# Kernel tuning notes

Measured on AMD Instinct MI355X. Metric: run time of the kernel, lower is better.

Reference implementation:

```python
import jax, jax.numpy as jnp
import numpy as np

NUM_EMBEDDINGS = 16384
EMBEDDING_DIM = 512
COMMITMENT_COST = 0.25  # legacy: vq_loss = commit + beta * codebook
NORM_EPS = 1e-12  # F.normalize default eps


def setup_inputs() -> dict:
    key = jax.random.key(0)
    k_z, k_emb, k_w, k_b = jax.random.split(key, 4)
    z = jax.random.normal(k_z, (8, 1024, EMBEDDING_DIM), dtype=jnp.float32)
    # frozen codebook, init normal with std = D^{-0.5}
    embedding_weight = jax.random.normal(k_emb, (NUM_EMBEDDINGS, EMBEDDING_DIM), dtype=jnp.float32) * (EMBEDDING_DIM ** -0.5)
    # learnable projection (torch Linear: y = x @ W.T + b, W is [out, in])
    bound = 1.0 / np.sqrt(EMBEDDING_DIM)
    proj_w = jax.random.uniform(k_w, (EMBEDDING_DIM, EMBEDDING_DIM), dtype=jnp.float32, minval=-bound, maxval=bound)
    proj_b = jax.random.uniform(k_b, (EMBEDDING_DIM,), dtype=jnp.float32, minval=-bound, maxval=bound)
    scale = jnp.asarray(10.0, dtype=jnp.float32)
    return {"z": z, "embedding_weight": embedding_weight, "proj_w": proj_w, "proj_b": proj_b, "scale": scale}


def _l2_normalize(x):
    n = jnp.linalg.norm(x, axis=-1, keepdims=True)
    return x / jnp.maximum(n, NORM_EPS)


def reference(z, embedding_weight, proj_w, proj_b, scale):
    B, N, D = z.shape
    z_flat = z.reshape(-1, D)                                   # [M, D]
    quant_codebook = embedding_weight @ proj_w.T + proj_b       # [K, D]
    z_n = _l2_normalize(z_flat)
    c_n = _l2_normalize(quant_codebook)
    distances = -(z_n @ c_n.T) * scale                          # [M, K]
    encoding_indices = jnp.argmin(distances, axis=1)            # [M]
    quantized = quant_codebook[encoding_indices].reshape(z.shape)
    commitment_loss = jnp.mean((jax.lax.stop_gradient(quantized) - z) ** 2)
    codebook_loss = jnp.mean((quantized - jax.lax.stop_gradient(z)) ** 2)
    vq_loss = commitment_loss + COMMITMENT_COST * codebook_loss  # legacy=True
    quantized = z + jax.lax.stop_gradient(quantized - z)         # straight-through
    encoding_indices = encoding_indices.reshape(B, N)
    return quantized, vq_loss, encoding_indices
```

## Files before the change

kernel.cpp:

```cpp
#include <hip/hip_runtime.h>
#include <math.h>


typedef _Float16 f16;
typedef _Float16 f16x8 __attribute__((ext_vector_type(8)));
typedef _Float16 f16x4 __attribute__((ext_vector_type(4)));
typedef short s16x8 __attribute__((ext_vector_type(8)));
typedef float f32x4 __attribute__((ext_vector_type(4)));
typedef unsigned int u32;
typedef unsigned long long u64;
typedef unsigned short ushort_t;

#define INV2048 (1.0f/2048.0f)
#define MARGIN  0.010f

#define OFF_Q    0u
#define OFF_EHI  33554432u
#define OFF_ELO  50331648u
#define OFF_WHI  67108864u
#define OFF_WLO  67633152u
#define OFF_CB   68157440u
#define OFF_ZB   84934656u
#define OFF_RL   93323264u
#define OFF_PK   OFF_EHI

__device__ __forceinline__ void gload_lds16(const void* g, void* l) {
  __builtin_amdgcn_global_load_lds(
      (const __attribute__((address_space(1))) u32*)g,
      (__attribute__((address_space(3))) u32*)l, 16, 0, 0);
}

__device__ __forceinline__ void stage_tile(const void* __restrict__ src, int row0,
                                           int kt, char* lds, int tid) {
#pragma unroll
  for (int i = 0; i < 4; ++i) {
    int lin = i * 256 + tid;
    int row = lin >> 3;
    int slot = lin & 7;
    int k8 = slot ^ (row & 7);
    const char* g = (const char*)src + (((size_t)(row0 + row)) << 10)
                    + (size_t)(kt * 128 + k8 * 16);
    gload_lds16(g, lds + lin * 16);
  }
}

__device__ __forceinline__ u64 make_key(float v, int idx) {
  u32 b = __float_as_uint(v);
  u32 m = (u32)((int)b >> 31) | 0x80000000u;
  return ((u64)(b ^ m) << 32) | (u32)(0x7FFFFFFF - idx);
}
__device__ __forceinline__ float key_val(u64 k) {
  u32 o = (u32)(k >> 32);
  u32 m = (o & 0x80000000u) ? 0x80000000u : 0xFFFFFFFFu;
  return __uint_as_float(o ^ m);
}
__device__ __forceinline__ int key_idx(u64 k) {
  return 0x7FFFFFFF - (int)(u32)(k & 0xFFFFFFFFu);
}
__device__ __forceinline__ u64 umax64(u64 a, u64 b) { return a > b ? a : b; }

#define LDS_AHI 0
#define LDS_ALO 16384
#define LDS_BHI 32768
#define LDS_BLO 49152

__global__ __launch_bounds__(256, 2) void k_gemm_codebook(
    const f16* __restrict__ Ahi, const f16* __restrict__ Alo,
    const f16* __restrict__ Bhi, const f16* __restrict__ Blo,
    const float* __restrict__ bias, float* __restrict__ Q) {
  __shared__ __align__(16) char lds[65536];
  f32x4 hh[4][4], xx[4][4];
  const int tid = threadIdx.x;
  const int m0 = blockIdx.y * 128;
  const int n0 = blockIdx.x * 128;
  const int l = tid & 63;
  const int wid = tid >> 6;
  const int wr = (wid >> 1) * 64;
  const int wc = (wid & 1) * 64;
  const int r7 = (l & 15) & 7;

#pragma unroll
  for (int a = 0; a < 4; ++a)
#pragma unroll
    for (int b = 0; b < 4; ++b) {
      hh[a][b] = (f32x4){0.f, 0.f, 0.f, 0.f};
      xx[a][b] = (f32x4){0.f, 0.f, 0.f, 0.f};
    }

  for (int kt = 0; kt < 8; ++kt) {
    stage_tile(Ahi, m0, kt, lds + LDS_AHI, tid);
    stage_tile(Alo, m0, kt, lds + LDS_ALO, tid);
    stage_tile(Bhi, n0, kt, lds + LDS_BHI, tid);
    stage_tile(Blo, n0, kt, lds + LDS_BLO, tid);
    __syncthreads();
#pragma unroll
    for (int ks = 0; ks < 2; ++ks) {
      const int kg = ks * 4 + (l >> 4);
      const int s = (kg ^ r7) * 16;
      const char* pa = lds + (wr + (l & 15)) * 128 + s;
      const char* pb = lds + (wc + (l & 15)) * 128 + s;
      f16x8 ahi[4], alo[4];
#pragma unroll
      for (int mf = 0; mf < 4; ++mf) {
        ahi[mf] = *(const f16x8*)(pa + LDS_AHI + mf * 2048);
        alo[mf] = *(const f16x8*)(pa + LDS_ALO + mf * 2048);
      }
#pragma unroll
      for (int nf = 0; nf < 4; ++nf) {
        f16x8 bhi = *(const f16x8*)(pb + LDS_BHI + nf * 2048);
        f16x8 blo = *(const f16x8*)(pb + LDS_BLO + nf * 2048);
#pragma unroll
        for (int mf = 0; mf < 4; ++mf) {
          hh[mf][nf] = __builtin_amdgcn_mfma_f32_16x16x32_f16(ahi[mf], bhi, hh[mf][nf], 0, 0, 0);
          xx[mf][nf] = __builtin_amdgcn_mfma_f32_16x16x32_f16(ahi[mf], blo, xx[mf][nf], 0, 0, 0);
          xx[mf][nf] = __builtin_amdgcn_mfma_f32_16x16x32_f16(alo[mf], bhi, xx[mf][nf], 0, 0, 0);
        }
      }
    }
    __syncthreads();
  }

#pragma unroll
  for (int mf = 0; mf < 4; ++mf)
#pragma unroll
    for (int nf = 0; nf < 4; ++nf)
#pragma unroll
      for (int j = 0; j < 4; ++j) {
        int row = m0 + wr + mf * 16 + (l >> 4) * 4 + j;
        int col = n0 + wc + nf * 16 + (l & 15);
        Q[(size_t)row * 512 + col] = hh[mf][nf][j] + xx[mf][nf][j] * INV2048 + bias[col];
      }
}

__global__ __launch_bounds__(256, 4) void k_gemm_coarse(
    const ushort_t* __restrict__ CB, const ushort_t* __restrict__ ZB,
    u64* __restrict__ pk) {
  __shared__ __align__(16) char lds[32768];
  f32x4 acc[4][4];
  const int tid = threadIdx.x;
  const int cb0 = blockIdx.x * 128;
  const int zb0 = blockIdx.y * 128;
  const int l = tid & 63;
  const int wid = tid >> 6;
  const int wr = (wid >> 1);
  const int wc = (wid & 1);
  const int r7 = (l & 15) & 7;

#pragma unroll
  for (int a = 0; a < 4; ++a)
#pragma unroll
    for (int b = 0; b < 4; ++b) acc[a][b] = (f32x4){0.f, 0.f, 0.f, 0.f};

  for (int kt = 0; kt < 8; ++kt) {
    stage_tile(CB, cb0, kt, lds, tid);
    stage_tile(ZB, zb0, kt, lds + 16384, tid);
    __syncthreads();
#pragma unroll
    for (int ks = 0; ks < 2; ++ks) {
      const int kg = ks * 4 + (l >> 4);
      const int s = (kg ^ r7) * 16;
      const char* pa = lds + (wr * 64 + (l & 15)) * 128 + s;
      const char* pb = lds + 16384 + (wc * 64 + (l & 15)) * 128 + s;
      s16x8 af[4];
#pragma unroll
      for (int mf = 0; mf < 4; ++mf)
        af[mf] = *(const s16x8*)(pa + mf * 2048);
#pragma unroll
      for (int nf = 0; nf < 4; ++nf) {
        s16x8 bf = *(const s16x8*)(pb + nf * 2048);
#pragma unroll
        for (int mf = 0; mf < 4; ++mf)
          acc[mf][nf] = __builtin_amdgcn_mfma_f32_16x16x32_bf16(af[mf], bf, acc[mf][nf], 0, 0, 0);
      }
    }
    __syncthreads();
  }

  float* cmax = (float*)lds;
  u32* cnt = (u32*)(lds + 1024);
  u64* slots = (u64*)(lds + 2048);

  float cm[4];
#pragma unroll
  for (int nf = 0; nf < 4; ++nf) {
    float m = acc[0][nf][0];
#pragma unroll
    for (int mf = 0; mf < 4; ++mf)
#pragma unroll
      for (int j = 0; j < 4; ++j) m = fmaxf(m, acc[mf][nf][j]);
    m = fmaxf(m, __shfl_xor(m, 16, 64));
    m = fmaxf(m, __shfl_xor(m, 32, 64));
    cm[nf] = m;
  }
  if (tid < 128) cnt[tid] = 0;
  slots[tid] = 0;
  slots[tid + 256] = 0;
  if ((l >> 4) == 0) {
#pragma unroll
    for (int nf = 0; nf < 4; ++nf)
      cmax[(wc * 64 + nf * 16 + l) * 2 + wr] = cm[nf];
  }
  __syncthreads();

#pragma unroll
  for (int nf = 0; nf < 4; ++nf) {
    int col = wc * 64 + nf * 16 + (l & 15);
    float thresh = fmaxf(cmax[col * 2], cmax[col * 2 + 1]) - MARGIN;
#pragma unroll
    for (int mf = 0; mf < 4; ++mf)
#pragma unroll
      for (int j = 0; j < 4; ++j) {
        float v = acc[mf][nf][j];
        if (v >= thresh) {
          int code = cb0 + wr * 64 + mf * 16 + ((l >> 4) << 2) + j;
          u32 p = atomicAdd(&cnt[col], 1u);
          if (p < 4) slots[col * 4 + p] = make_key(v, code);
        }
      }
  }
  __syncthreads();

  if (tid < 128) {
    size_t base = (((size_t)(zb0 + tid)) * 128 + blockIdx.x) * 4;
#pragma unroll
    for (int s = 0; s < 4; ++s) pk[base + s] = slots[tid * 4 + s];
  }
}

__global__ __launch_bounds__(256) void k_split(const float* __restrict__ src,
                                               f16* __restrict__ hi,
                                               f16* __restrict__ lo, int n4) {
  int i = blockIdx.x * 256 + threadIdx.x;
  if (i >= n4) return;
  const float4 v = ((const float4*)src)[i];
  f16 h0 = (f16)v.x, h1 = (f16)v.y, h2 = (f16)v.z, h3 = (f16)v.w;
  ((f16x4*)hi)[i] = (f16x4){h0, h1, h2, h3};
  ((f16x4*)lo)[i] = (f16x4){(f16)((v.x - (float)h0) * 2048.0f),
                            (f16)((v.y - (float)h1) * 2048.0f),
                            (f16)((v.z - (float)h2) * 2048.0f),
                            (f16)((v.w - (float)h3) * 2048.0f)};
}

__device__ __forceinline__ ushort_t f2bf_rne(float f) {
  u32 b = __float_as_uint(f);
  b += 0x7FFFu + ((b >> 16) & 1u);
  return (ushort_t)(b >> 16);
}

__global__ __launch_bounds__(256) void k_norm_bf16(const float* __restrict__ src,
                                                   ushort_t* __restrict__ dst) {
  __shared__ float red[256];
  const int row = blockIdx.x, t = threadIdx.x;
  float q0 = src[(size_t)row * 512 + t];
  float q1 = src[(size_t)row * 512 + t + 256];
  red[t] = q0 * q0 + q1 * q1;
  __syncthreads();
  for (int s = 128; s > 0; s >>= 1) {
    if (t < s) red[t] += red[t + s];
    __syncthreads();
  }
  float inv = 1.0f / fmaxf(sqrtf(red[0]), 1e-12f);
  dst[(size_t)row * 512 + t] = f2bf_rne(q0 * inv);
  dst[(size_t)row * 512 + t + 256] = f2bf_rne(q1 * inv);
}

__global__ __launch_bounds__(256) void k_rescore_gather(
    const u64* __restrict__ pk, const float* __restrict__ Q,
    const float* __restrict__ z, float* __restrict__ outq,
    float* __restrict__ outidx, float* __restrict__ rloss) {
  __shared__ float sz[512];
  __shared__ double redd[8];
  __shared__ u64 redk[4];
  __shared__ int cand[64];
  __shared__ int ccount;
  const int row = blockIdx.x, t = threadIdx.x;

  sz[t] = z[(size_t)row * 512 + t];
  sz[t + 256] = z[(size_t)row * 512 + t + 256];
  if (t == 0) ccount = 0;

  u64 k1 = pk[(size_t)row * 512 + t * 2];
  u64 k2 = pk[(size_t)row * 512 + t * 2 + 1];
  u64 km = umax64(k1, k2);
  for (int m = 1; m < 64; m <<= 1)
    km = umax64(km, (u64)__shfl_xor((long long)km, m));
  if ((t & 63) == 0) redk[t >> 6] = km;
  __syncthreads();
  u64 gk = umax64(umax64(redk[0], redk[1]), umax64(redk[2], redk[3]));
  float thresh = key_val(gk) - MARGIN;

  if (key_val(k1) >= thresh) { int p = atomicAdd(&ccount, 1); if (p < 64) cand[p] = key_idx(k1); }
  if (key_val(k2) >= thresh) { int p = atomicAdd(&ccount, 1); if (p < 64) cand[p] = key_idx(k2); }
  __syncthreads();
  int nc = ccount < 64 ? ccount : 64;

  double bs = -1e300;
  int bi = 0x7FFFFFFF;
  for (int c = 0; c < nc; ++c) {
    int code = cand[c];
    const float* Qr = Q + (size_t)code * 512;
    double dotp = 0.0, qq = 0.0;
#pragma unroll
    for (int h = 0; h < 2; ++h) {
      int d = t + h * 256;
      double qv = (double)Qr[d];
      dotp += (double)sz[d] * qv;
      qq += qv * qv;
    }
    for (int m = 1; m < 64; m <<= 1) {
      dotp += __shfl_xor(dotp, m);
      qq += __shfl_xor(qq, m);
    }
    if ((t & 63) == 0) { redd[t >> 6] = dotp; redd[4 + (t >> 6)] = qq; }
    __syncthreads();
    double dsum = redd[0] + redd[1] + redd[2] + redd[3];
    double qsum = redd[4] + redd[5] + redd[6] + redd[7];
    double s = dsum / fmax(sqrt(qsum), 1e-12);
    if (s > bs || (s == bs && code < bi)) { bs = s; bi = code; }
    __syncthreads();
  }

  const float* Qb = Q + (size_t)bi * 512;
  double lsum = 0.0;
#pragma unroll
  for (int h = 0; h < 2; ++h) {
    int d = t + h * 256;
    float qv = Qb[d], zv = sz[d];
    outq[(size_t)row * 512 + d] = zv + (qv - zv);
    float df = qv - zv;
    lsum += (double)df * (double)df;
  }
  for (int m = 1; m < 64; m <<= 1) lsum += __shfl_xor(lsum, m);
  if ((t & 63) == 0) redd[t >> 6] = lsum;
  __syncthreads();
  if (t == 0) {
    rloss[row] = (float)(redd[0] + redd[1] + redd[2] + redd[3]);
    outidx[row] = (float)bi;
  }
}

__global__ __launch_bounds__(256) void k_loss_final(const float* __restrict__ rloss,
                                                    float* __restrict__ out_loss) {
  __shared__ float sl[256];
  int t = threadIdx.x;
  float s = 0.f;
#pragma unroll
  for (int i = 0; i < 32; ++i) s += rloss[t + i * 256];
  sl[t] = s;
  __syncthreads();
  for (int k = 128; k > 0; k >>= 1) {
    if (t < k) sl[t] += sl[t + k];
    __syncthreads();
  }
  if (t == 0) out_loss[0] = 1.25f * sl[0] / 4194304.0f;
}

extern "C" void kernel_launch(void* const* d_in, const int* in_sizes, int n_in,
                              void* d_out, int out_size, void* d_ws, size_t ws_size,
                              hipStream_t stream) {
  const float* z = (const float*)d_in[0];
  const float* emb = (const float*)d_in[1];
  const float* pw = (const float*)d_in[2];
  const float* pb = (const float*)d_in[3];

  char* ws = (char*)d_ws;
  float* Q = (float*)(ws + OFF_Q);
  f16* ehi = (f16*)(ws + OFF_EHI);
  f16* elo = (f16*)(ws + OFF_ELO);
  f16* whi = (f16*)(ws + OFF_WHI);
  f16* wlo = (f16*)(ws + OFF_WLO);
  ushort_t* cb = (ushort_t*)(ws + OFF_CB);
  ushort_t* zb = (ushort_t*)(ws + OFF_ZB);
  u64* pk = (u64*)(ws + OFF_PK);
  float* rloss = (float*)(ws + OFF_RL);

  float* outq = (float*)d_out;
  float* outloss = outq + 4194304;
  float* outidx = outq + 4194305;

  k_split<<<8192, 256, 0, stream>>>(emb, ehi, elo, 2097152);
  k_split<<<256, 256, 0, stream>>>(pw, whi, wlo, 65536);
  k_norm_bf16<<<8192, 256, 0, stream>>>(z, zb);
  k_gemm_codebook<<<dim3(4, 128), 256, 0, stream>>>(ehi, elo, whi, wlo, pb, Q);
  k_norm_bf16<<<16384, 256, 0, stream>>>(Q, cb);
  k_gemm_coarse<<<dim3(128, 64), 256, 0, stream>>>(cb, zb, pk);
  k_rescore_gather<<<8192, 256, 0, stream>>>(pk, Q, z, outq, outidx, rloss);
  k_loss_final<<<1, 256, 0, stream>>>(rloss, outloss);
}
```

Before: 286.1 us.

## Rewrite coarse similarity GEMM as 256x256 double-buffered 8-wave pipelined kernel

Replaces the 128x128 coarse bf16 GEMM with a 512-thread kernel using 256x256 tiles and double-buffered 128KB LDS. Global-to-LDS prefetch of the next k-slice is interleaved with MFMA phases, and s_setprio and partial vmcnt waits are used to overlap loads with compute and reduce barrier stalls. The larger tile halves the number of per-block candidate lists, so the rescore kernel now reads 256 candidate keys per row instead of 512. This relies on a new LDS layout without an XOR swizzle, which may cause bank conflicts. Lower occupancy and higher register pressure are also risks.

```diff
diff --git a/kernel.cpp b/kernel.cpp
--- a/kernel.cpp
+++ b/kernel.cpp
@@ -30,6 +30,26 @@
       (__attribute__((address_space(3))) u32*)l, 16, 0, 0);
 }
 
+__device__ __forceinline__ u64 make_key(float v, int idx) {
+  u32 b = __float_as_uint(v);
+  u32 m = (u32)((int)b >> 31) | 0x80000000u;
+  return ((u64)(b ^ m) << 32) | (u32)(0x7FFFFFFF - idx);
+}
+__device__ __forceinline__ float key_val(u64 k) {
+  u32 o = (u32)(k >> 32);
+  u32 m = (o & 0x80000000u) ? 0x80000000u : 0xFFFFFFFFu;
+  return __uint_as_float(o ^ m);
+}
+__device__ __forceinline__ int key_idx(u64 k) {
+  return 0x7FFFFFFF - (int)(u32)(k & 0xFFFFFFFFu);
+}
+__device__ __forceinline__ u64 umax64(u64 a, u64 b) { return a > b ? a : b; }
+
+#define LDS_AHI 0
+#define LDS_ALO 16384
+#define LDS_BHI 32768
+#define LDS_BLO 49152
+
 __device__ __forceinline__ void stage_tile(const void* __restrict__ src, int row0,
                                            int kt, char* lds, int tid) {
 #pragma unroll
@@ -43,26 +63,6 @@
     gload_lds16(g, lds + lin * 16);
   }
 }
-
-__device__ __forceinline__ u64 make_key(float v, int idx) {
-  u32 b = __float_as_uint(v);
-  u32 m = (u32)((int)b >> 31) | 0x80000000u;
-  return ((u64)(b ^ m) << 32) | (u32)(0x7FFFFFFF - idx);
-}
-__device__ __forceinline__ float key_val(u64 k) {
-  u32 o = (u32)(k >> 32);
-  u32 m = (o & 0x80000000u) ? 0x80000000u : 0xFFFFFFFFu;
-  return __uint_as_float(o ^ m);
-}
-__device__ __forceinline__ int key_idx(u64 k) {
-  return 0x7FFFFFFF - (int)(u32)(k & 0xFFFFFFFFu);
-}
-__device__ __forceinline__ u64 umax64(u64 a, u64 b) { return a > b ? a : b; }
-
-#define LDS_AHI 0
-#define LDS_ALO 16384
-#define LDS_BHI 32768
-#define LDS_BLO 49152
 
 __global__ __launch_bounds__(256, 2) void k_gemm_codebook(
     const f16* __restrict__ Ahi, const f16* __restrict__ Alo,
@@ -132,69 +132,109 @@
       }
 }
 
-__global__ __launch_bounds__(256, 4) void k_gemm_coarse(
+#define PHASE(CUR, KS, MFH, PF, STISA, STKS, WN)                               \
+  {                                                                            \
+    const char* base_ = lds + (CUR) * 65536 + (KS) * 16384;                    \
+    if ((MFH) == 0) {                                                          \
+      bfr[0] = *(const s16x8*)(base_ + boff + 0);                              \
+      bfr[1] = *(const s16x8*)(base_ + boff + 256);                            \
+      bfr[2] = *(const s16x8*)(base_ + boff + 512);                            \
+      bfr[3] = *(const s16x8*)(base_ + boff + 768);                            \
+    }                                                                          \
+    s16x8 af0 = *(const s16x8*)(base_ + aoff + (MFH) * 1024 + 0);              \
+    s16x8 af1 = *(const s16x8*)(base_ + aoff + (MFH) * 1024 + 256);            \
+    s16x8 af2 = *(const s16x8*)(base_ + aoff + (MFH) * 1024 + 512);            \
+    s16x8 af3 = *(const s16x8*)(base_ + aoff + (MFH) * 1024 + 768);            \
+    if (PF) {                                                                  \
+      char* d_ = lds + ((t & 1) ^ 1) * 65536 + ((STISA) ? 0 : 32768)           \
+                 + (STKS) * 16384 + tid * 16;                                  \
+      const char* g_ = ((STISA) ? srcA : srcB) + (t + 1) * 128 + (STKS) * 64;  \
+      gload_lds16(g_, d_);                                                     \
+      gload_lds16(g_ + 32, d_ + 8192);                                         \
+    }                                                                          \
+    __builtin_amdgcn_s_setprio(1);                                             \
+    _Pragma("unroll") for (int nf = 0; nf < 4; ++nf) {                         \
+      acc[(MFH)*4+0][nf] = __builtin_amdgcn_mfma_f32_16x16x32_bf16(af0, bfr[nf], acc[(MFH)*4+0][nf], 0, 0, 0); \
+      acc[(MFH)*4+1][nf] = __builtin_amdgcn_mfma_f32_16x16x32_bf16(af1, bfr[nf], acc[(MFH)*4+1][nf], 0, 0, 0); \
+      acc[(MFH)*4+2][nf] = __builtin_amdgcn_mfma_f32_16x16x32_bf16(af2, bfr[nf], acc[(MFH)*4+2][nf], 0, 0, 0); \
+      acc[(MFH)*4+3][nf] = __builtin_amdgcn_mfma_f32_16x16x32_bf16(af3, bfr[nf], acc[(MFH)*4+3][nf], 0, 0, 0); \
+    }                                                                          \
+    __builtin_amdgcn_s_setprio(0);                                             \
+    asm volatile("s_waitcnt vmcnt(" #WN ")\n\ts_barrier" ::: "memory");        \
+  }
+
+__global__ __launch_bounds__(512, 2) void k_gemm_coarse8(
     const ushort_t* __restrict__ CB, const ushort_t* __restrict__ ZB,
     u64* __restrict__ pk) {
-  __shared__ __align__(16) char lds[32768];
-  f32x4 acc[4][4];
+  __shared__ __align__(16) char lds[131072];
   const int tid = threadIdx.x;
-  const int cb0 = blockIdx.x * 128;
-  const int zb0 = blockIdx.y * 128;
   const int l = tid & 63;
   const int wid = tid >> 6;
-  const int wr = (wid >> 1);
-  const int wc = (wid & 1);
-  const int r7 = (l & 15) & 7;
-
-#pragma unroll
-  for (int a = 0; a < 4; ++a)
+  const int wr = wid >> 2;
+  const int wc = wid & 3;
+  const int cb0 = blockIdx.x * 256;
+  const int zb0 = blockIdx.y * 256;
+
+  const int srow = tid & 255, skg = tid >> 8;
+  const char* srcA = (const char*)CB + (((size_t)(cb0 + srow)) << 10) + skg * 16;
+  const char* srcB = (const char*)ZB + (((size_t)(zb0 + srow)) << 10) + skg * 16;
+
+  const int lane_off = (l >> 4) * 4096 + (l & 15) * 16;
+  const int aoff = wr * 2048 + lane_off;
+  const int boff = 32768 + wc * 1024 + lane_off;
+
+  f32x4 acc[8][4];
+#pragma unroll
+  for (int a = 0; a < 8; ++a)
 #pragma unroll
     for (int b = 0; b < 4; ++b) acc[a][b] = (f32x4){0.f, 0.f, 0.f, 0.f};
 
-  for (int kt = 0; kt < 8; ++kt) {
-    stage_tile(CB, cb0, kt, lds, tid);
-    stage_tile(ZB, zb0, kt, lds + 16384, tid);
-    __syncthreads();
-#pragma unroll
-    for (int ks = 0; ks < 2; ++ks) {
-      const int kg = ks * 4 + (l >> 4);
-      const int s = (kg ^ r7) * 16;
-      const char* pa = lds + (wr * 64 + (l & 15)) * 128 + s;
-      const char* pb = lds + 16384 + (wc * 64 + (l & 15)) * 128 + s;
-      s16x8 af[4];
-#pragma unroll
-      for (int mf = 0; mf < 4; ++mf)
-        af[mf] = *(const s16x8*)(pa + mf * 2048);
-#pragma unroll
-      for (int nf = 0; nf < 4; ++nf) {
-        s16x8 bf = *(const s16x8*)(pb + nf * 2048);
-#pragma unroll
-        for (int mf = 0; mf < 4; ++mf)
-          acc[mf][nf] = __builtin_amdgcn_mfma_f32_16x16x32_bf16(af[mf], bf, acc[mf][nf], 0, 0, 0);
-      }
-    }
-    __syncthreads();
+  {
+    char* d;
+    const char* g;
+    d = lds + 0 + tid * 16;        g = srcA + 0;         gload_lds16(g, d); gload_lds16(g + 32, d + 8192);
+    d = lds + 32768 + tid * 16;    g = srcB + 0;         gload_lds16(g, d); gload_lds16(g + 32, d + 8192);
+    d = lds + 16384 + tid * 16;    g = srcA + 64;        gload_lds16(g, d); gload_lds16(g + 32, d + 8192);
+    d = lds + 49152 + tid * 16;    g = srcB + 64;        gload_lds16(g, d); gload_lds16(g + 32, d + 8192);
+    asm volatile("s_waitcnt vmcnt(4)\n\ts_barrier" ::: "memory");
+  }
+
+  s16x8 bfr[4];
+  for (int t = 0; t < 7; ++t) {
+    const int cur = t & 1;
+    PHASE(cur, 0, 0, true, 1, 0, 4)
+    PHASE(cur, 0, 1, true, 0, 0, 4)
+    PHASE(cur, 1, 0, true, 1, 1, 4)
+    PHASE(cur, 1, 1, true, 0, 1, 4)
+  }
+  {
+    const int t = 7;
+    (void)t;
+    PHASE(1, 0, 0, false, 1, 0, 2)
+    PHASE(1, 0, 1, false, 0, 0, 0)
+    PHASE(1, 1, 0, false, 1, 1, 0)
+    PHASE(1, 1, 1, false, 0, 1, 0)
   }
 
   float* cmax = (float*)lds;
-  u32* cnt = (u32*)(lds + 1024);
-  u64* slots = (u64*)(lds + 2048);
+  u32* cnt = (u32*)(lds + 2048);
+  u64* slots = (u64*)(lds + 4096);
 
   float cm[4];
 #pragma unroll
   for (int nf = 0; nf < 4; ++nf) {
     float m = acc[0][nf][0];
 #pragma unroll
-    for (int mf = 0; mf < 4; ++mf)
-#pragma unroll
-      for (int j = 0; j < 4; ++j) m = fmaxf(m, acc[mf][nf][j]);
+    for (int mfa = 0; mfa < 8; ++mfa)
+#pragma unroll
+      for (int j = 0; j < 4; ++j) m = fmaxf(m, acc[mfa][nf][j]);
     m = fmaxf(m, __shfl_xor(m, 16, 64));
     m = fmaxf(m, __shfl_xor(m, 32, 64));
     cm[nf] = m;
   }
-  if (tid < 128) cnt[tid] = 0;
+  if (tid < 256) cnt[tid] = 0;
   slots[tid] = 0;
-  slots[tid + 256] = 0;
+  slots[tid + 512] = 0;
   if ((l >> 4) == 0) {
 #pragma unroll
     for (int nf = 0; nf < 4; ++nf)
@@ -207,12 +247,12 @@
     int col = wc * 64 + nf * 16 + (l & 15);
     float thresh = fmaxf(cmax[col * 2], cmax[col * 2 + 1]) - MARGIN;
 #pragma unroll
-    for (int mf = 0; mf < 4; ++mf)
+    for (int mfa = 0; mfa < 8; ++mfa)
 #pragma unroll
       for (int j = 0; j < 4; ++j) {
-        float v = acc[mf][nf][j];
+        float v = acc[mfa][nf][j];
         if (v >= thresh) {
-          int code = cb0 + wr * 64 + mf * 16 + ((l >> 4) << 2) + j;
+          int code = cb0 + wr * 128 + mfa * 16 + ((l >> 4) << 2) + j;
           u32 p = atomicAdd(&cnt[col], 1u);
           if (p < 4) slots[col * 4 + p] = make_key(v, code);
         }
@@ -220,8 +260,8 @@
   }
   __syncthreads();
 
-  if (tid < 128) {
-    size_t base = (((size_t)(zb0 + tid)) * 128 + blockIdx.x) * 4;
+  if (tid < 256) {
+    size_t base = (((size_t)(zb0 + tid)) * 64 + blockIdx.x) * 4;
 #pragma unroll
     for (int s = 0; s < 4; ++s) pk[base + s] = slots[tid * 4 + s];
   }
@@ -279,9 +319,8 @@
   sz[t + 256] = z[(size_t)row * 512 + t + 256];
   if (t == 0) ccount = 0;
 
-  u64 k1 = pk[(size_t)row * 512 + t * 2];
-  u64 k2 = pk[(size_t)row * 512 + t * 2 + 1];
-  u64 km = umax64(k1, k2);
+  u64 k1 = pk[(size_t)row * 256 + t];
+  u64 km = k1;
   for (int m = 1; m < 64; m <<= 1)
     km = umax64(km, (u64)__shfl_xor((long long)km, m));
   if ((t & 63) == 0) redk[t >> 6] = km;
@@ -290,7 +329,6 @@
   float thresh = key_val(gk) - MARGIN;
 
   if (key_val(k1) >= thresh) { int p = atomicAdd(&ccount, 1); if (p < 64) cand[p] = key_idx(k1); }
-  if (key_val(k2) >= thresh) { int p = atomicAdd(&ccount, 1); if (p < 64) cand[p] = key_idx(k2); }
   __syncthreads();
   int nc = ccount < 64 ? ccount : 64;
 
@@ -383,7 +421,7 @@
   k_norm_bf16<<<8192, 256, 0, stream>>>(z, zb);
   k_gemm_codebook<<<dim3(4, 128), 256, 0, stream>>>(ehi, elo, whi, wlo, pb, Q);
   k_norm_bf16<<<16384, 256, 0, stream>>>(Q, cb);
-  k_gemm_coarse<<<dim3(128, 64), 256, 0, stream>>>(cb, zb, pk);
+  k_gemm_coarse8<<<dim3(64, 32), 512, 0, stream>>>(cb, zb, pk);
   k_rescore_gather<<<8192, 256, 0, stream>>>(pk, Q, z, outq, outidx, rloss);
   k_loss_final<<<1, 256, 0, stream>>>(rloss, outloss);
 }
```

Measured after the change: 352.8 us. 1.23x slower.

## Rewrite coarse similarity GEMM with 256x256 tiles and double-buffered pipelined LDS

Applied to the files above, without the earlier changes.

The coarse bf16 similarity GEMM moves from 128x128 tiles with 256 threads to 256x256 tiles with 512 threads. It double-buffers a 128KB LDS staging area with interleaved half-tile prefetches, uses barrier-separated MFMA phases with s_setprio, and applies a grid swizzle for L2 locality. Each block now keeps 4 candidates per 256 codes instead of per 128, which halves the candidate buffer the rescore kernel reads. The aim is more data reuse per load and memory latency hidden behind MFMA work. The cost is lower occupancy and fewer candidate slots per code range, which could drop near-ties.

```diff
diff --git a/kernel.cpp b/kernel.cpp
--- a/kernel.cpp
+++ b/kernel.cpp
@@ -30,6 +30,26 @@
       (__attribute__((address_space(3))) u32*)l, 16, 0, 0);
 }
 
+__device__ __forceinline__ u64 make_key(float v, int idx) {
+  u32 b = __float_as_uint(v);
+  u32 m = (u32)((int)b >> 31) | 0x80000000u;
+  return ((u64)(b ^ m) << 32) | (u32)(0x7FFFFFFF - idx);
+}
+__device__ __forceinline__ float key_val(u64 k) {
+  u32 o = (u32)(k >> 32);
+  u32 m = (o & 0x80000000u) ? 0x80000000u : 0xFFFFFFFFu;
+  return __uint_as_float(o ^ m);
+}
+__device__ __forceinline__ int key_idx(u64 k) {
+  return 0x7FFFFFFF - (int)(u32)(k & 0xFFFFFFFFu);
+}
+__device__ __forceinline__ u64 umax64(u64 a, u64 b) { return a > b ? a : b; }
+
+#define LDS_AHI 0
+#define LDS_ALO 16384
+#define LDS_BHI 32768
+#define LDS_BLO 49152
+
 __device__ __forceinline__ void stage_tile(const void* __restrict__ src, int row0,
                                            int kt, char* lds, int tid) {
 #pragma unroll
@@ -43,26 +63,6 @@
     gload_lds16(g, lds + lin * 16);
   }
 }
-
-__device__ __forceinline__ u64 make_key(float v, int idx) {
-  u32 b = __float_as_uint(v);
-  u32 m = (u32)((int)b >> 31) | 0x80000000u;
-  return ((u64)(b ^ m) << 32) | (u32)(0x7FFFFFFF - idx);
-}
-__device__ __forceinline__ float key_val(u64 k) {
-  u32 o = (u32)(k >> 32);
-  u32 m = (o & 0x80000000u) ? 0x80000000u : 0xFFFFFFFFu;
-  return __uint_as_float(o ^ m);
-}
-__device__ __forceinline__ int key_idx(u64 k) {
-  return 0x7FFFFFFF - (int)(u32)(k & 0xFFFFFFFFu);
-}
-__device__ __forceinline__ u64 umax64(u64 a, u64 b) { return a > b ? a : b; }
-
-#define LDS_AHI 0
-#define LDS_ALO 16384
-#define LDS_BHI 32768
-#define LDS_BLO 49152
 
 __global__ __launch_bounds__(256, 2) void k_gemm_codebook(
     const f16* __restrict__ Ahi, const f16* __restrict__ Alo,
@@ -132,87 +132,146 @@
       }
 }
 
-__global__ __launch_bounds__(256, 4) void k_gemm_coarse(
+#define BAR() __builtin_amdgcn_s_barrier()
+
+#define STAGE_HALF(TT, HW)                                                     \
+  {                                                                            \
+    const char* g0_ = (((HW) >> 1) ? srcZ : srcC)                              \
+                      + (((HW) & 1) ? 131072 : 0) + (TT) * 128;                \
+    char* d0_ = lds + ((TT) & 1) * 65536 + ((HW) >> 1) * 32768                 \
+                + ((HW) & 1) * 16384;                                          \
+    gload_lds16(g0_ + goff0, d0_ + doff0);                                     \
+    gload_lds16(g0_ + goff1, d0_ + doff1);                                     \
+  }
+
+#define LDA(MH)                                                                \
+  _Pragma("unroll") for (int mfi_ = 0; mfi_ < 4; ++mfi_) {                     \
+    a[mfi_][0] = *(const s16x8*)(lds + buf + abase + (MH) * 16384 + mfi_ * 2048 + sk0); \
+    a[mfi_][1] = *(const s16x8*)(lds + buf + abase + (MH) * 16384 + mfi_ * 2048 + sk1); \
+  }
+#define LDB(NH)                                                                \
+  _Pragma("unroll") for (int nfi_ = 0; nfi_ < 2; ++nfi_) {                     \
+    b[NH][nfi_][0] = *(const s16x8*)(lds + buf + bbase + (NH) * 16384 + nfi_ * 2048 + sk0); \
+    b[NH][nfi_][1] = *(const s16x8*)(lds + buf + bbase + (NH) * 16384 + nfi_ * 2048 + sk1); \
+  }
+
+#define MM(AB, NH)                                                             \
+  __builtin_amdgcn_s_setprio(1);                                               \
+  _Pragma("unroll") for (int nfi_ = 0; nfi_ < 2; ++nfi_)                       \
+  _Pragma("unroll") for (int mfi_ = 0; mfi_ < 4; ++mfi_) {                     \
+    acc[(AB) + mfi_][(NH) * 2 + nfi_] = __builtin_amdgcn_mfma_f32_16x16x32_bf16( \
+        a[mfi_][0], b[NH][nfi_][0], acc[(AB) + mfi_][(NH) * 2 + nfi_], 0, 0, 0); \
+    acc[(AB) + mfi_][(NH) * 2 + nfi_] = __builtin_amdgcn_mfma_f32_16x16x32_bf16( \
+        a[mfi_][1], b[NH][nfi_][1], acc[(AB) + mfi_][(NH) * 2 + nfi_], 0, 0, 0); \
+  }                                                                            \
+  __builtin_amdgcn_s_setprio(0);
+
+__global__ __launch_bounds__(512, 2) void k_gemm_coarse8(
     const ushort_t* __restrict__ CB, const ushort_t* __restrict__ ZB,
     u64* __restrict__ pk) {
-  __shared__ __align__(16) char lds[32768];
-  f32x4 acc[4][4];
+  __shared__ __align__(16) char lds[131072];
   const int tid = threadIdx.x;
-  const int cb0 = blockIdx.x * 128;
-  const int zb0 = blockIdx.y * 128;
   const int l = tid & 63;
   const int wid = tid >> 6;
-  const int wr = (wid >> 1);
-  const int wc = (wid & 1);
-  const int r7 = (l & 15) & 7;
-
-#pragma unroll
-  for (int a = 0; a < 4; ++a)
-#pragma unroll
-    for (int b = 0; b < 4; ++b) acc[a][b] = (f32x4){0.f, 0.f, 0.f, 0.f};
-
-  for (int kt = 0; kt < 8; ++kt) {
-    stage_tile(CB, cb0, kt, lds, tid);
-    stage_tile(ZB, zb0, kt, lds + 16384, tid);
-    __syncthreads();
-#pragma unroll
-    for (int ks = 0; ks < 2; ++ks) {
-      const int kg = ks * 4 + (l >> 4);
-      const int s = (kg ^ r7) * 16;
-      const char* pa = lds + (wr * 64 + (l & 15)) * 128 + s;
-      const char* pb = lds + 16384 + (wc * 64 + (l & 15)) * 128 + s;
-      s16x8 af[4];
-#pragma unroll
-      for (int mf = 0; mf < 4; ++mf)
-        af[mf] = *(const s16x8*)(pa + mf * 2048);
-#pragma unroll
-      for (int nf = 0; nf < 4; ++nf) {
-        s16x8 bf = *(const s16x8*)(pb + nf * 2048);
-#pragma unroll
-        for (int mf = 0; mf < 4; ++mf)
-          acc[mf][nf] = __builtin_amdgcn_mfma_f32_16x16x32_bf16(af[mf], bf, acc[mf][nf], 0, 0, 0);
-      }
-    }
-    __syncthreads();
-  }
+  const int wr = wid >> 2;
+  const int wc = wid & 3;
+  const int id = blockIdx.x;
+  const int swz = (id & 7) * 256 + (id >> 3);
+  const int cbx = swz & 63, zby = swz >> 6;
+  const int cb0 = cbx * 256, zb0 = zby * 256;
+
+  const int lin0 = wid * 128 + l;
+  const int lin1 = lin0 + 64;
+  const u32 goff0 = (u32)((lin0 >> 3) * 1024 + (((lin0 & 7) ^ ((lin0 >> 3) & 7)) * 16));
+  const u32 goff1 = (u32)((lin1 >> 3) * 1024 + (((lin1 & 7) ^ ((lin1 >> 3) & 7)) * 16));
+  const u32 doff0 = (u32)lin0 * 16;
+  const u32 doff1 = (u32)lin1 * 16;
+  const char* srcC = (const char*)CB + ((size_t)cb0 << 10);
+  const char* srcZ = (const char*)ZB + ((size_t)zb0 << 10);
+
+  const int r7 = l & 7;
+  const u32 sk0 = (u32)(((l >> 4) ^ r7) * 16);
+  const u32 sk1 = (u32)((((l >> 4) | 4) ^ r7) * 16);
+  const u32 abase = (u32)(wr * 8192 + (l & 15) * 128);
+  const u32 bbase = (u32)(32768 + wc * 4096 + (l & 15) * 128);
+
+  f32x4 acc[8][4];
+#pragma unroll
+  for (int x = 0; x < 8; ++x)
+#pragma unroll
+    for (int y = 0; y < 4; ++y) acc[x][y] = (f32x4){0.f, 0.f, 0.f, 0.f};
+  s16x8 a[4][2];
+  s16x8 b[2][2][2];
+
+  STAGE_HALF(0, 0) STAGE_HALF(0, 1) STAGE_HALF(0, 2) STAGE_HALF(0, 3)
+  STAGE_HALF(1, 0) STAGE_HALF(1, 2) STAGE_HALF(1, 3)
+  asm volatile("s_waitcnt vmcnt(6)" ::: "memory");
+  BAR();
+
+#pragma unroll
+  for (int g = 0; g < 8; ++g) {
+    const u32 buf = (u32)(g & 1) * 65536u;
+    LDA(0) LDB(0)
+    if (g < 7) STAGE_HALF(g + 1, 1)
+    BAR();
+    MM(0, 0)
+    BAR();
+    LDB(1)
+    if (g < 6) STAGE_HALF(g + 2, 0)
+    BAR();
+    MM(0, 1)
+    BAR();
+    LDA(1)
+    if (g < 6) STAGE_HALF(g + 2, 2)
+    BAR();
+    MM(4, 1)
+    BAR();
+    if (g < 6) STAGE_HALF(g + 2, 3)
+    BAR();
+    MM(4, 0)
+    if (g < 6) { asm volatile("s_waitcnt vmcnt(6)" ::: "memory"); }
+    else if (g == 6) { asm volatile("s_waitcnt vmcnt(0)" ::: "memory"); }
+    BAR();
+  }
+  __syncthreads();
 
   float* cmax = (float*)lds;
-  u32* cnt = (u32*)(lds + 1024);
-  u64* slots = (u64*)(lds + 2048);
+  u32* cnt = (u32*)(lds + 2048);
+  u64* slots = (u64*)(lds + 4096);
 
   float cm[4];
 #pragma unroll
-  for (int nf = 0; nf < 4; ++nf) {
-    float m = acc[0][nf][0];
-#pragma unroll
-    for (int mf = 0; mf < 4; ++mf)
-#pragma unroll
-      for (int j = 0; j < 4; ++j) m = fmaxf(m, acc[mf][nf][j]);
+  for (int N = 0; N < 4; ++N) {
+    float m = acc[0][N][0];
+#pragma unroll
+    for (int A = 0; A < 8; ++A)
+#pragma unroll
+      for (int j = 0; j < 4; ++j) m = fmaxf(m, acc[A][N][j]);
     m = fmaxf(m, __shfl_xor(m, 16, 64));
     m = fmaxf(m, __shfl_xor(m, 32, 64));
-    cm[nf] = m;
-  }
-  if (tid < 128) cnt[tid] = 0;
+    cm[N] = m;
+  }
+  if (tid < 256) cnt[tid] = 0;
   slots[tid] = 0;
-  slots[tid + 256] = 0;
+  slots[tid + 512] = 0;
   if ((l >> 4) == 0) {
 #pragma unroll
-    for (int nf = 0; nf < 4; ++nf)
-      cmax[(wc * 64 + nf * 16 + l) * 2 + wr] = cm[nf];
-  }
-  __syncthreads();
-
-#pragma unroll
-  for (int nf = 0; nf < 4; ++nf) {
-    int col = wc * 64 + nf * 16 + (l & 15);
+    for (int N = 0; N < 4; ++N)
+      cmax[((N >> 1) * 128 + wc * 32 + (N & 1) * 16 + l) * 2 + wr] = cm[N];
+  }
+  __syncthreads();
+
+#pragma unroll
+  for (int N = 0; N < 4; ++N) {
+    int col = (N >> 1) * 128 + wc * 32 + (N & 1) * 16 + (l & 15);
     float thresh = fmaxf(cmax[col * 2], cmax[col * 2 + 1]) - MARGIN;
 #pragma unroll
-    for (int mf = 0; mf < 4; ++mf)
+    for (int A = 0; A < 8; ++A)
 #pragma unroll
       for (int j = 0; j < 4; ++j) {
-        float v = acc[mf][nf][j];
+        float v = acc[A][N][j];
         if (v >= thresh) {
-          int code = cb0 + wr * 64 + mf * 16 + ((l >> 4) << 2) + j;
+          int code = cb0 + (A >> 2) * 128 + wr * 64 + (A & 3) * 16 + ((l >> 4) << 2) + j;
           u32 p = atomicAdd(&cnt[col], 1u);
           if (p < 4) slots[col * 4 + p] = make_key(v, code);
         }
@@ -220,8 +279,8 @@
   }
   __syncthreads();
 
-  if (tid < 128) {
-    size_t base = (((size_t)(zb0 + tid)) * 128 + blockIdx.x) * 4;
+  if (tid < 256) {
+    size_t base = (((size_t)(zb0 + tid)) * 64 + cbx) * 4;
 #pragma unroll
     for (int s = 0; s < 4; ++s) pk[base + s] = slots[tid * 4 + s];
   }
@@ -279,9 +338,8 @@
   sz[t + 256] = z[(size_t)row * 512 + t + 256];
   if (t == 0) ccount = 0;
 
-  u64 k1 = pk[(size_t)row * 512 + t * 2];
-  u64 k2 = pk[(size_t)row * 512 + t * 2 + 1];
-  u64 km = umax64(k1, k2);
+  u64 k1 = pk[(size_t)row * 256 + t];
+  u64 km = k1;
   for (int m = 1; m < 64; m <<= 1)
     km = umax64(km, (u64)__shfl_xor((long long)km, m));
   if ((t & 63) == 0) redk[t >> 6] = km;
@@ -290,7 +348,6 @@
   float thresh = key_val(gk) - MARGIN;
 
   if (key_val(k1) >= thresh) { int p = atomicAdd(&ccount, 1); if (p < 64) cand[p] = key_idx(k1); }
-  if (key_val(k2) >= thresh) { int p = atomicAdd(&ccount, 1); if (p < 64) cand[p] = key_idx(k2); }
   __syncthreads();
   int nc = ccount < 64 ? ccount : 64;
 
@@ -383,7 +440,7 @@
   k_norm_bf16<<<8192, 256, 0, stream>>>(z, zb);
   k_gemm_codebook<<<dim3(4, 128), 256, 0, stream>>>(ehi, elo, whi, wlo, pb, Q);
   k_norm_bf16<<<16384, 256, 0, stream>>>(Q, cb);
-  k_gemm_coarse<<<dim3(128, 64), 256, 0, stream>>>(cb, zb, pk);
+  k_gemm_coarse8<<<2048, 512, 0, stream>>>(cb, zb, pk);
   k_rescore_gather<<<8192, 256, 0, stream>>>(pk, Q, z, outq, outidx, rloss);
   k_loss_final<<<1, 256, 0, stream>>>(rloss, outloss);
 }
```

Measured after the change: 298.6 us. 4.4% more time.

## Double-buffer coarse GEMM K loop with direct global-to-LDS loads

Applied to the files above, without the earlier changes.

Restructures the coarse bf16 GEMM main loop from 8 K-tiles of 64 with a full stage-then-compute-then-sync cycle into 16 K-tiles of 32 using two LDS buffers. The next tile is issued via gload_lds16 (global-to-LDS loads) while the current tile is computed, with a new XOR swizzle for the 64-byte rows. The goal is to hide global memory latency and cut one barrier per iteration. The trade-off is more, smaller iterations and reliance on the async LDS load path being ordered correctly by the single barrier.

```diff
diff --git a/kernel.cpp b/kernel.cpp
--- a/kernel.cpp
+++ b/kernel.cpp
@@ -144,37 +144,58 @@
   const int wid = tid >> 6;
   const int wr = (wid >> 1);
   const int wc = (wid & 1);
-  const int r7 = (l & 15) & 7;
+
+  const int rA0 = tid >> 2, sA0 = tid & 3;
+  const int rA1 = (tid + 256) >> 2, sA1 = tid & 3;
+  const u32 ga0 = (u32)(rA0 * 1024 + ((sA0 ^ (rA0 & 3)) * 16));
+  const u32 ga1 = (u32)(rA1 * 1024 + ((sA1 ^ (rA1 & 3)) * 16));
+  const char* gA = (const char*)CB + ((size_t)cb0 << 10);
+  const char* gB = (const char*)ZB + ((size_t)zb0 << 10);
+  const u32 d0 = (u32)tid * 16;
+  const u32 d1 = d0 + 4096;
+
+#define STAGE32(KT, BUF)                                                       \
+  {                                                                            \
+    char* db_ = lds + (BUF) * 16384;                                           \
+    const u32 ko_ = (u32)(KT) * 64;                                            \
+    gload_lds16(gA + ga0 + ko_, db_ + d0);                                     \
+    gload_lds16(gA + ga1 + ko_, db_ + d1);                                     \
+    gload_lds16(gB + ga0 + ko_, db_ + 8192 + d0);                              \
+    gload_lds16(gB + ga1 + ko_, db_ + 8192 + d1);                              \
+  }
+
+  const u32 sphys = (u32)((((l >> 4)) ^ ((l & 15) & 3)) * 16);
+  const u32 aoff = (u32)((wr * 64 + (l & 15)) * 64) + sphys;
+  const u32 boff = 8192u + (u32)((wc * 64 + (l & 15)) * 64) + sphys;
 
 #pragma unroll
   for (int a = 0; a < 4; ++a)
 #pragma unroll
     for (int b = 0; b < 4; ++b) acc[a][b] = (f32x4){0.f, 0.f, 0.f, 0.f};
 
-  for (int kt = 0; kt < 8; ++kt) {
-    stage_tile(CB, cb0, kt, lds, tid);
-    stage_tile(ZB, zb0, kt, lds + 16384, tid);
-    __syncthreads();
-#pragma unroll
-    for (int ks = 0; ks < 2; ++ks) {
-      const int kg = ks * 4 + (l >> 4);
-      const int s = (kg ^ r7) * 16;
-      const char* pa = lds + (wr * 64 + (l & 15)) * 128 + s;
-      const char* pb = lds + 16384 + (wc * 64 + (l & 15)) * 128 + s;
-      s16x8 af[4];
-#pragma unroll
-      for (int mf = 0; mf < 4; ++mf)
-        af[mf] = *(const s16x8*)(pa + mf * 2048);
-#pragma unroll
-      for (int nf = 0; nf < 4; ++nf) {
-        s16x8 bf = *(const s16x8*)(pb + nf * 2048);
-#pragma unroll
-        for (int mf = 0; mf < 4; ++mf)
-          acc[mf][nf] = __builtin_amdgcn_mfma_f32_16x16x32_bf16(af[mf], bf, acc[mf][nf], 0, 0, 0);
-      }
-    }
-    __syncthreads();
-  }
+#define COMPUTE32(BUF)                                                         \
+  {                                                                            \
+    const char* base_ = lds + (BUF) * 16384;                                   \
+    s16x8 af[4];                                                               \
+    _Pragma("unroll") for (int mf = 0; mf < 4; ++mf)                           \
+      af[mf] = *(const s16x8*)(base_ + aoff + mf * 1024);                      \
+    _Pragma("unroll") for (int nf = 0; nf < 4; ++nf) {                         \
+      s16x8 bf = *(const s16x8*)(base_ + boff + nf * 1024);                    \
+      _Pragma("unroll") for (int mf = 0; mf < 4; ++mf)                         \
+        acc[mf][nf] = __builtin_amdgcn_mfma_f32_16x16x32_bf16(af[mf], bf, acc[mf][nf], 0, 0, 0); \
+    }                                                                          \
+  }
+
+  STAGE32(0, 0)
+  __syncthreads();
+#pragma unroll 2
+  for (int kt = 0; kt < 15; ++kt) {
+    STAGE32(kt + 1, (kt & 1) ^ 1)
+    COMPUTE32(kt & 1)
+    __syncthreads();
+  }
+  COMPUTE32(1)
+  __syncthreads();
 
   float* cmax = (float*)lds;
   u32* cnt = (u32*)(lds + 1024);
@@ -225,6 +246,8 @@
 #pragma unroll
     for (int s = 0; s < 4; ++s) pk[base + s] = slots[tid * 4 + s];
   }
+#undef STAGE32
+#undef COMPUTE32
 }
 
 __global__ __launch_bounds__(256) void k_split(const float* __restrict__ src,
```

Measured after the change: 307.6 us. +7.5%, slower.
